# Optimization experiments

Measured on AMD Instinct MI355X. Metric: run time of the kernel, lower is better.

## Reference

```python
import jax, jax.numpy as jnp
import numpy as np

ALPHA = 1.702   # SwiGLU alpha
LIMIT = 7.0     # swiglu_limit clamp
EPS = 1e-5      # RMSNorm eps
TOPK = 4        # experts_per_token
CHUNK = 8       # token chunk for gathered-weight einsum (bounds memory)


def _swiglu(h):
    # h: (..., 2*I) with interleaved [glu, linear] pairs
    g = jnp.minimum(h[..., ::2], LIMIT)
    l = jnp.clip(h[..., 1::2], -LIMIT, LIMIT)
    return g * jax.nn.sigmoid(ALPHA * g) * (l + 1.0)


def setup_inputs() -> dict:
    key = jax.random.key(0)
    ks = jax.random.split(key, 5)
    T, H, I, E = 1024, 1024, 1024, 64
    s = 0.02
    return {
        "x": jax.random.normal(ks[0], (T, H), jnp.float32),
        "norm_scale": jnp.ones((H,), jnp.float32),
        "gate_w": jax.random.normal(ks[1], (E, H), jnp.float32) * s,
        "gate_b": jnp.zeros((E,), jnp.float32),
        "mlp1_w": jax.random.normal(ks[2], (E, 2 * I, H), jnp.float32) * s,
        "mlp1_b": jnp.zeros((E, 2 * I), jnp.float32),
        "mlp2_w": jax.random.normal(ks[3], (E, H, I), jnp.float32) * s,
        "mlp2_b": jnp.zeros((E, H), jnp.float32),
    }


def reference(x, norm_scale, gate_w, gate_b, mlp1_w, mlp1_b, mlp2_w, mlp2_b):
    # RMSNorm (fp32 math)
    t = x * jax.lax.rsqrt(jnp.mean(x * x, axis=-1, keepdims=True) + EPS) * norm_scale
    # gating: top-k over gate logits, softmax over the k selected
    logits = t @ gate_w.T + gate_b                     # (T, E)
    vals, idx = jax.lax.top_k(logits, TOPK)            # sorted desc, matches torch.topk(sorted=True)
    ew = jax.nn.softmax(vals, axis=-1)                 # (T, k)

    T_, H = t.shape
    nc = T_ // CHUNK

    @jax.checkpoint
    def per_chunk(args):
        xc, ic, wc = args                              # (C,H), (C,k), (C,k)
        h = jnp.einsum('bekh,bh->bek', mlp1_w[ic], xc) + mlp1_b[ic]   # (C,k,2I)
        h = _swiglu(h)                                                 # (C,k,I)
        o = jnp.einsum('behi,bei->beh', mlp2_w[ic], h) + mlp2_b[ic]    # (C,k,H)
        return jnp.einsum('beh,be->bh', o, wc)                         # (C,H)

    out = jax.lax.map(per_chunk, (t.reshape(nc, CHUNK, H),
                                  idx.reshape(nc, CHUNK, TOPK),
                                  ew.reshape(nc, CHUNK, TOPK)))
    return x + out.reshape(T_, H)
```

## Files before the change

### kernel.cpp

```cpp
#include <hip/hip_runtime.h>
#include <hip/hip_bf16.h>

#define GLOBAL_AS __attribute__((address_space(1)))
#define LDS_AS    __attribute__((address_space(3)))

typedef __bf16 bf16x8 __attribute__((ext_vector_type(8)));
typedef float  f32x4v __attribute__((ext_vector_type(4)));

__device__ __forceinline__ unsigned short f2bf(float f) {
    union { float f; unsigned int u; } a; a.f = f;
    unsigned int u = a.u;
    u += 0x7FFFu + ((u >> 16) & 1u);
    return (unsigned short)(u >> 16);
}

__global__ __launch_bounds__(256) void k_rmsnorm(const float* __restrict__ x,
        const float* __restrict__ sc, float* __restrict__ t32,
        unsigned short* __restrict__ t16)
{
    const int t = blockIdx.x, tid = threadIdx.x;
    const float4 v = ((const float4*)(x + (size_t)t * 1024))[tid];
    float ss = v.x*v.x + v.y*v.y + v.z*v.z + v.w*v.w;
    #pragma unroll
    for (int s = 32; s; s >>= 1) ss += __shfl_xor(ss, s, 64);
    __shared__ float red[4];
    if ((tid & 63) == 0) red[tid >> 6] = ss;
    __syncthreads();
    const float tot = red[0] + red[1] + red[2] + red[3];
    const float rs = rsqrtf(tot * (1.0f / 1024.0f) + 1e-5f);
    const float4 s4 = ((const float4*)sc)[tid];
    float4 o;
    o.x = v.x * rs * s4.x; o.y = v.y * rs * s4.y;
    o.z = v.z * rs * s4.z; o.w = v.w * rs * s4.w;
    ((float4*)(t32 + (size_t)t * 1024))[tid] = o;
    uint2 p;
    p.x = (unsigned)f2bf(o.x) | ((unsigned)f2bf(o.y) << 16);
    p.y = (unsigned)f2bf(o.z) | ((unsigned)f2bf(o.w) << 16);
    ((uint2*)(t16 + (size_t)t * 1024))[tid] = p;
}

__global__ __launch_bounds__(64) void k_gate(const float* __restrict__ t32,
        const float* __restrict__ gw, const float* __restrict__ gb,
        int* __restrict__ idx, float* __restrict__ ew)
{
    const int t = blockIdx.x, tid = threadIdx.x;
    __shared__ float4 tl[256];
    __shared__ float lg[64];
    const float4* xr = (const float4*)(t32 + (size_t)t * 1024);
    #pragma unroll
    for (int i = 0; i < 4; ++i) tl[i * 64 + tid] = xr[i * 64 + tid];
    __syncthreads();
    const float4* w4 = (const float4*)(gw + (size_t)tid * 1024);
    float acc = gb[tid];
    for (int k = 0; k < 256; ++k) {
        const float4 a = tl[k], b = w4[k];
        acc += a.x*b.x; acc += a.y*b.y; acc += a.z*b.z; acc += a.w*b.w;
    }
    lg[tid] = acc;
    __syncthreads();
    if (tid == 0) {
        unsigned long long taken = 0ull;
        float vals[4]; int ids[4];
        for (int k = 0; k < 4; ++k) {
            float bv = -3.0e38f; int bi = 0;
            for (int e = 0; e < 64; ++e) {
                if ((taken >> e) & 1ull) continue;
                if (lg[e] > bv) { bv = lg[e]; bi = e; }
            }
            taken |= 1ull << bi; vals[k] = bv; ids[k] = bi;
        }
        float ex[4], s = 0.0f;
        for (int k = 0; k < 4; ++k) { ex[k] = expf(vals[k] - vals[0]); s += ex[k]; }
        const float inv = 1.0f / s;
        for (int k = 0; k < 4; ++k) { idx[t*4+k] = ids[k]; ew[t*4+k] = ex[k] * inv; }
    }
}

__global__ __launch_bounds__(256) void k_bucket(const int* __restrict__ idx,
        const float* __restrict__ ewv, int* __restrict__ eoff,
        int* __restrict__ slot_token, float* __restrict__ slot_ew,
        int* __restrict__ token_slots)
{
    __shared__ int cnt[64], cur[64];
    const int tid = threadIdx.x;
    if (tid < 64) cnt[tid] = 0;
    __syncthreads();
    for (int p = tid; p < 4096; p += 256) atomicAdd(&cnt[idx[p]], 1);
    __syncthreads();
    if (tid == 0) {
        int s = 0;
        for (int e = 0; e < 64; ++e) { eoff[e] = s; cur[e] = s; s += cnt[e]; }
        eoff[64] = s;
    }
    __syncthreads();
    for (int p = tid; p < 4096; p += 256) {
        const int e = idx[p];
        const int s = atomicAdd(&cur[e], 1);
        slot_token[s] = p >> 2;
        slot_ew[s] = ewv[p];
        token_slots[p] = s;
    }
}

template<int MODE>
__global__ __launch_bounds__(256, 2) void k_gemm(
        const float* __restrict__ W, const float* __restrict__ Bias,
        const unsigned short* __restrict__ A,
        const int* __restrict__ eoff, const int* __restrict__ slot_token,
        const float* __restrict__ slot_ew,
        unsigned short* __restrict__ act_out, float* __restrict__ o_buf)
{
    constexpr int NPE = (MODE == 0) ? 2048 : 1024;
    const int e  = blockIdx.y;
    const int nt = blockIdx.x;
    const int off = eoff[e];
    const int count = eoff[e + 1] - off;
    if (count == 0) return;
    const int tid = threadIdx.x;
    const int wv = tid >> 6, l = tid & 63;
    const int wm = wv >> 1, wn = wv & 1;

    __shared__ unsigned char lds[2][32768];

    const float* Wb = W + (size_t)e * NPE * 1024 + (size_t)nt * 128 * 1024;

    for (int mt = 0; mt * 128 < count; ++mt) {
        const unsigned char* asrc[4];
        #pragma unroll
        for (int i = 0; i < 4; ++i) {
            const int chunk = wv * 4 + i;
            const int row = chunk * 8 + (l >> 3);
            const int colbyte = ((l & 7) ^ (l >> 3)) << 4;
            int arow;
            if (MODE == 0) {
                int slot = off + mt * 128 + row;
                const int smax = off + count - 1;
                if (slot > smax) slot = smax;
                arow = slot_token[slot];
            } else {
                arow = off + mt * 128 + row;
            }
            asrc[i] = (const unsigned char*)A + (size_t)arow * 2048 + colbyte;
        }

        f32x4v acc[4][4];
        #pragma unroll
        for (int m = 0; m < 4; ++m)
            #pragma unroll
            for (int n = 0; n < 4; ++n)
                acc[m][n] = f32x4v{0.f, 0.f, 0.f, 0.f};

        float4 bv[8];

        #pragma unroll
        for (int i = 0; i < 4; ++i)
            __builtin_amdgcn_global_load_lds((const GLOBAL_AS void*)asrc[i],
                (LDS_AS void*)&lds[0][(wv * 4 + i) * 1024], 16, 0, 0);
        #pragma unroll
        for (int it = 0; it < 8; ++it) {
            const int fid = it * 256 + tid;
            bv[it] = *(const float4*)(Wb + (size_t)(fid >> 4) * 1024 + (fid & 15) * 4);
        }
        #pragma unroll
        for (int it = 0; it < 8; ++it) {
            const int fid = it * 256 + tid;
            const int row = fid >> 4, c4 = fid & 15;
            uint2 p;
            p.x = (unsigned)f2bf(bv[it].x) | ((unsigned)f2bf(bv[it].y) << 16);
            p.y = (unsigned)f2bf(bv[it].z) | ((unsigned)f2bf(bv[it].w) << 16);
            *(uint2*)(&lds[0][16384 + row * 128 + ((c4 * 8) ^ ((row & 7) << 4))]) = p;
        }
        __syncthreads();

        int buf = 0;
        for (int kt = 0; kt < 16; ++kt) {
            const bool pf = (kt < 15);
            if (pf) {
                #pragma unroll
                for (int i = 0; i < 4; ++i)
                    __builtin_amdgcn_global_load_lds(
                        (const GLOBAL_AS void*)(asrc[i] + (kt + 1) * 128),
                        (LDS_AS void*)&lds[buf ^ 1][(wv * 4 + i) * 1024], 16, 0, 0);
                #pragma unroll
                for (int it = 0; it < 8; ++it) {
                    const int fid = it * 256 + tid;
                    bv[it] = *(const float4*)(Wb + (size_t)(fid >> 4) * 1024
                                              + (kt + 1) * 64 + (fid & 15) * 4);
                }
            }
            #pragma unroll
            for (int kk = 0; kk < 2; ++kk) {
                bf16x8 af[4], bfr[4];
                #pragma unroll
                for (int m = 0; m < 4; ++m) {
                    const int row = wm * 64 + m * 16 + (l & 15);
                    af[m] = *(const bf16x8*)(&lds[buf][row * 128 +
                              ((kk * 64 + ((l >> 4) * 16)) ^ ((row & 7) << 4))]);
                }
                #pragma unroll
                for (int n = 0; n < 4; ++n) {
                    const int row = wn * 64 + n * 16 + (l & 15);
                    bfr[n] = *(const bf16x8*)(&lds[buf][16384 + row * 128 +
                              ((kk * 64 + ((l >> 4) * 16)) ^ ((row & 7) << 4))]);
                }
                #pragma unroll
                for (int m = 0; m < 4; ++m)
                    #pragma unroll
                    for (int n = 0; n < 4; ++n)
                        acc[m][n] = __builtin_amdgcn_mfma_f32_16x16x32_bf16(
                                        af[m], bfr[n], acc[m][n], 0, 0, 0);
            }
            if (pf) {
                #pragma unroll
                for (int it = 0; it < 8; ++it) {
                    const int fid = it * 256 + tid;
                    const int row = fid >> 4, c4 = fid & 15;
                    uint2 p;
                    p.x = (unsigned)f2bf(bv[it].x) | ((unsigned)f2bf(bv[it].y) << 16);
                    p.y = (unsigned)f2bf(bv[it].z) | ((unsigned)f2bf(bv[it].w) << 16);
                    *(uint2*)(&lds[buf ^ 1][16384 + row * 128 +
                              ((c4 * 8) ^ ((row & 7) << 4))]) = p;
                }
            }
            __syncthreads();
            buf ^= 1;
        }

        #pragma unroll
        for (int m = 0; m < 4; ++m) {
            #pragma unroll
            for (int n = 0; n < 4; ++n) {
                #pragma unroll
                for (int j = 0; j < 4; ++j) {
                    const int row  = wm * 64 + m * 16 + (l >> 4) * 4 + j;
                    const int coll = wn * 64 + n * 16 + (l & 15);
                    const int gn = nt * 128 + coll;
                    const int gm = mt * 128 + row;
                    if (MODE == 0) {
                        float v = acc[m][n][j] + Bias[(size_t)e * NPE + gn];
                        const float partner = __shfl_xor(v, 1, 64);
                        if (!(l & 1) && gm < count) {
                            const float g  = fminf(v, 7.0f);
                            const float lv = fminf(fmaxf(partner, -7.0f), 7.0f);
                            const float r  = g / (1.0f + expf(-1.702f * g)) * (lv + 1.0f);
                            act_out[(size_t)(off + gm) * 1024 + (gn >> 1)] = f2bf(r);
                        }
                    } else {
                        if (gm < count) {
                            const int slot = off + gm;
                            const float v = acc[m][n][j] + Bias[(size_t)e * NPE + gn];
                            o_buf[(size_t)slot * 1024 + gn] = v * slot_ew[slot];
                        }
                    }
                }
            }
        }
    }
}

__global__ __launch_bounds__(256) void k_combine(const float* __restrict__ x,
        const float* __restrict__ o_buf, const int* __restrict__ tslot,
        float* __restrict__ out)
{
    const int t = blockIdx.x, tid = threadIdx.x;
    float4 r = ((const float4*)(x + (size_t)t * 1024))[tid];
    #pragma unroll
    for (int k = 0; k < 4; ++k) {
        const int s = tslot[t * 4 + k];
        const float4 o = ((const float4*)(o_buf + (size_t)s * 1024))[tid];
        r.x += o.x; r.y += o.y; r.z += o.z; r.w += o.w;
    }
    ((float4*)(out + (size_t)t * 1024))[tid] = r;
}

extern "C" void kernel_launch(void* const* d_in, const int* in_sizes, int n_in,
                              void* d_out, int out_size, void* d_ws, size_t ws_size,
                              hipStream_t stream)
{
    const float* x   = (const float*)d_in[0];
    const float* nsc = (const float*)d_in[1];
    const float* gw  = (const float*)d_in[2];
    const float* gb  = (const float*)d_in[3];
    const float* w1  = (const float*)d_in[4];
    const float* b1  = (const float*)d_in[5];
    const float* w2  = (const float*)d_in[6];
    const float* b2  = (const float*)d_in[7];
    float* out = (float*)d_out;
    (void)in_sizes; (void)n_in; (void)out_size; (void)ws_size;

    char* ws = (char*)d_ws;
    float*          t32   = (float*)(ws);
    unsigned short* t16   = (unsigned short*)(ws + (4u  << 20));
    unsigned short* act   = (unsigned short*)(ws + (6u  << 20));
    float*          obuf  = (float*)(ws + (16u << 20));
    int*            idx   = (int*)  (ws + (32u << 20));
    float*          ew    = (float*)(ws + (32u << 20) + 1 * 65536);
    int*            stok  = (int*)  (ws + (32u << 20) + 2 * 65536);
    float*          sew   = (float*)(ws + (32u << 20) + 3 * 65536);
    int*            tslot = (int*)  (ws + (32u << 20) + 4 * 65536);
    int*            eoff  = (int*)  (ws + (32u << 20) + 5 * 65536);

    k_rmsnorm<<<1024, 256, 0, stream>>>(x, nsc, t32, t16);
    k_gate   <<<1024,  64, 0, stream>>>(t32, gw, gb, idx, ew);
    k_bucket <<<   1, 256, 0, stream>>>(idx, ew, eoff, stok, sew, tslot);
    k_gemm<0><<<dim3(16, 64), 256, 0, stream>>>(w1, b1, t16, eoff, stok, sew, act, nullptr);
    k_gemm<1><<<dim3( 8, 64), 256, 0, stream>>>(w2, b2, act, eoff, stok, sew, nullptr, obuf);
    k_combine<<<1024, 256, 0, stream>>>(x, obuf, tslot, out);
}
```

Baseline: 294.7 us.

## Deepen GEMM weight prefetch pipeline and parallelize gating top-k across waves

The expert GEMM main loop is unrolled by two and keeps two register buffers of fp32 weights, so weight loads run two K-tiles ahead. Explicit sched_barrier and s_waitcnt calls control the overlap of the A-tile DMA into LDS, the B loads, the MFMA work and the LDS writes. The gating kernel moves to 256 threads with a split-K dot product and a wave-wide shuffle/ballot top-k in place of a serial single-thread scan. Manual bf16 rounding is replaced by native __bf16 conversion. The risks are higher register pressure from the doubled prefetch buffers, and redundant clamped loads past the last K tile.

```diff
diff --git a/kernel.cpp b/kernel.cpp
--- a/kernel.cpp
+++ b/kernel.cpp
@@ -5,18 +5,12 @@
 #define LDS_AS    __attribute__((address_space(3)))
 
 typedef __bf16 bf16x8 __attribute__((ext_vector_type(8)));
+typedef __bf16 bf16x4 __attribute__((ext_vector_type(4)));
 typedef float  f32x4v __attribute__((ext_vector_type(4)));
-
-__device__ __forceinline__ unsigned short f2bf(float f) {
-    union { float f; unsigned int u; } a; a.f = f;
-    unsigned int u = a.u;
-    u += 0x7FFFu + ((u >> 16) & 1u);
-    return (unsigned short)(u >> 16);
-}
 
 __global__ __launch_bounds__(256) void k_rmsnorm(const float* __restrict__ x,
         const float* __restrict__ sc, float* __restrict__ t32,
-        unsigned short* __restrict__ t16)
+        __bf16* __restrict__ t16)
 {
     const int t = blockIdx.x, tid = threadIdx.x;
     const float4 v = ((const float4*)(x + (size_t)t * 1024))[tid];
@@ -33,46 +27,48 @@
     o.x = v.x * rs * s4.x; o.y = v.y * rs * s4.y;
     o.z = v.z * rs * s4.z; o.w = v.w * rs * s4.w;
     ((float4*)(t32 + (size_t)t * 1024))[tid] = o;
-    uint2 p;
-    p.x = (unsigned)f2bf(o.x) | ((unsigned)f2bf(o.y) << 16);
-    p.y = (unsigned)f2bf(o.z) | ((unsigned)f2bf(o.w) << 16);
-    ((uint2*)(t16 + (size_t)t * 1024))[tid] = p;
-}
-
-__global__ __launch_bounds__(64) void k_gate(const float* __restrict__ t32,
+    bf16x4 p;
+    p[0] = (__bf16)o.x; p[1] = (__bf16)o.y; p[2] = (__bf16)o.z; p[3] = (__bf16)o.w;
+    ((bf16x4*)(t16 + (size_t)t * 1024))[tid] = p;
+}
+
+__global__ __launch_bounds__(256) void k_gate(const float* __restrict__ t32,
         const float* __restrict__ gw, const float* __restrict__ gb,
         int* __restrict__ idx, float* __restrict__ ew)
 {
     const int t = blockIdx.x, tid = threadIdx.x;
     __shared__ float4 tl[256];
-    __shared__ float lg[64];
-    const float4* xr = (const float4*)(t32 + (size_t)t * 1024);
-    #pragma unroll
-    for (int i = 0; i < 4; ++i) tl[i * 64 + tid] = xr[i * 64 + tid];
-    __syncthreads();
-    const float4* w4 = (const float4*)(gw + (size_t)tid * 1024);
-    float acc = gb[tid];
-    for (int k = 0; k < 256; ++k) {
-        const float4 a = tl[k], b = w4[k];
-        acc += a.x*b.x; acc += a.y*b.y; acc += a.z*b.z; acc += a.w*b.w;
-    }
-    lg[tid] = acc;
-    __syncthreads();
-    if (tid == 0) {
-        unsigned long long taken = 0ull;
+    __shared__ float part[4][64];
+    tl[tid] = ((const float4*)(t32 + (size_t)t * 1024))[tid];
+    __syncthreads();
+    const int q = tid >> 6, e = tid & 63;
+    const float4* w4 = (const float4*)(gw + (size_t)e * 1024 + q * 256);
+    const float4* a4 = &tl[q * 64];
+    float acc = 0.0f;
+    #pragma unroll 8
+    for (int i = 0; i < 64; ++i) {
+        const float4 a = a4[i], b = w4[i];
+        acc += a.x*b.x + a.y*b.y + a.z*b.z + a.w*b.w;
+    }
+    part[q][e] = acc;
+    __syncthreads();
+    if (tid < 64) {
+        float cur = part[0][tid] + part[1][tid] + part[2][tid] + part[3][tid] + gb[tid];
         float vals[4]; int ids[4];
+        #pragma unroll
         for (int k = 0; k < 4; ++k) {
-            float bv = -3.0e38f; int bi = 0;
-            for (int e = 0; e < 64; ++e) {
-                if ((taken >> e) & 1ull) continue;
-                if (lg[e] > bv) { bv = lg[e]; bi = e; }
-            }
-            taken |= 1ull << bi; vals[k] = bv; ids[k] = bi;
+            float m = cur;
+            #pragma unroll
+            for (int s = 32; s; s >>= 1) m = fmaxf(m, __shfl_xor(m, s, 64));
+            const unsigned long long b = __ballot(cur == m);
+            const int bi = __ffsll(b) - 1;
+            vals[k] = m; ids[k] = bi;
+            if (tid == bi) cur = -3.0e38f;
         }
         float ex[4], s = 0.0f;
+        #pragma unroll
         for (int k = 0; k < 4; ++k) { ex[k] = expf(vals[k] - vals[0]); s += ex[k]; }
-        const float inv = 1.0f / s;
-        for (int k = 0; k < 4; ++k) { idx[t*4+k] = ids[k]; ew[t*4+k] = ex[k] * inv; }
+        if (tid < 4) { idx[t * 4 + tid] = ids[tid]; ew[t * 4 + tid] = ex[tid] / s; }
     }
 }
 
@@ -105,10 +101,10 @@
 template<int MODE>
 __global__ __launch_bounds__(256, 2) void k_gemm(
         const float* __restrict__ W, const float* __restrict__ Bias,
-        const unsigned short* __restrict__ A,
+        const __bf16* __restrict__ A,
         const int* __restrict__ eoff, const int* __restrict__ slot_token,
         const float* __restrict__ slot_ew,
-        unsigned short* __restrict__ act_out, float* __restrict__ o_buf)
+        __bf16* __restrict__ act_out, float* __restrict__ o_buf)
 {
     constexpr int NPE = (MODE == 0) ? 2048 : 1024;
     const int e  = blockIdx.y;
@@ -120,9 +116,63 @@
     const int wv = tid >> 6, l = tid & 63;
     const int wm = wv >> 1, wn = wv & 1;
 
-    __shared__ unsigned char lds[2][32768];
+    __shared__ __attribute__((aligned(16))) unsigned char lds[2][32768];
 
     const float* Wb = W + (size_t)e * NPE * 1024 + (size_t)nt * 128 * 1024;
+
+#define DMA_A(sbuf, kt) do {                                                   \
+    const int kk_ = (kt) > 15 ? 15 : (kt);                                     \
+    _Pragma("unroll")                                                          \
+    for (int i_ = 0; i_ < 4; ++i_)                                             \
+        __builtin_amdgcn_global_load_lds(                                      \
+            (const GLOBAL_AS void*)(asrc[i_] + kk_ * 128),                     \
+            (LDS_AS void*)&lds[sbuf][(wv * 4 + i_) * 1024], 16, 0, 0);         \
+    } while (0)
+
+#define LOAD_B(dst, kt) do {                                                   \
+    const int kk_ = (kt) > 15 ? 15 : (kt);                                     \
+    _Pragma("unroll")                                                          \
+    for (int it_ = 0; it_ < 8; ++it_) {                                        \
+        const int fid_ = it_ * 256 + tid;                                      \
+        dst[it_] = *(const float4*)(Wb + (size_t)(fid_ >> 4) * 1024            \
+                                    + kk_ * 64 + (fid_ & 15) * 4);             \
+    } } while (0)
+
+#define WRITE_B(src, sbuf) do {                                                \
+    _Pragma("unroll")                                                          \
+    for (int it_ = 0; it_ < 8; ++it_) {                                        \
+        const int fid_ = it_ * 256 + tid;                                      \
+        const int row_ = fid_ >> 4, c4_ = fid_ & 15;                           \
+        bf16x4 p_;                                                             \
+        p_[0] = (__bf16)src[it_].x; p_[1] = (__bf16)src[it_].y;                \
+        p_[2] = (__bf16)src[it_].z; p_[3] = (__bf16)src[it_].w;                \
+        *(bf16x4*)(&lds[sbuf][16384 + row_ * 128 +                             \
+                   ((c4_ * 8) ^ ((row_ & 7) << 4))]) = p_;                     \
+    } } while (0)
+
+#define COMPUTE(cbuf) do {                                                     \
+    _Pragma("unroll")                                                          \
+    for (int kk_ = 0; kk_ < 2; ++kk_) {                                        \
+        bf16x8 af_[4], bf_[4];                                                 \
+        _Pragma("unroll")                                                      \
+        for (int m_ = 0; m_ < 4; ++m_) {                                       \
+            const int row_ = wm * 64 + m_ * 16 + (l & 15);                     \
+            af_[m_] = *(const bf16x8*)(&lds[cbuf][row_ * 128 +                 \
+                      ((kk_ * 64 + ((l >> 4) * 16)) ^ ((row_ & 7) << 4))]);    \
+        }                                                                      \
+        _Pragma("unroll")                                                      \
+        for (int n_ = 0; n_ < 4; ++n_) {                                       \
+            const int row_ = wn * 64 + n_ * 16 + (l & 15);                     \
+            bf_[n_] = *(const bf16x8*)(&lds[cbuf][16384 + row_ * 128 +         \
+                      ((kk_ * 64 + ((l >> 4) * 16)) ^ ((row_ & 7) << 4))]);    \
+        }                                                                      \
+        _Pragma("unroll")                                                      \
+        for (int m_ = 0; m_ < 4; ++m_)                                         \
+            _Pragma("unroll")                                                  \
+            for (int n_ = 0; n_ < 4; ++n_)                                     \
+                acc[m_][n_] = __builtin_amdgcn_mfma_f32_16x16x32_bf16(         \
+                                  af_[m_], bf_[n_], acc[m_][n_], 0, 0, 0);     \
+    } } while (0)
 
     for (int mt = 0; mt * 128 < count; ++mt) {
         const unsigned char* asrc[4];
@@ -150,80 +200,39 @@
             for (int n = 0; n < 4; ++n)
                 acc[m][n] = f32x4v{0.f, 0.f, 0.f, 0.f};
 
-        float4 bv[8];
-
-        #pragma unroll
-        for (int i = 0; i < 4; ++i)
-            __builtin_amdgcn_global_load_lds((const GLOBAL_AS void*)asrc[i],
-                (LDS_AS void*)&lds[0][(wv * 4 + i) * 1024], 16, 0, 0);
-        #pragma unroll
-        for (int it = 0; it < 8; ++it) {
-            const int fid = it * 256 + tid;
-            bv[it] = *(const float4*)(Wb + (size_t)(fid >> 4) * 1024 + (fid & 15) * 4);
-        }
-        #pragma unroll
-        for (int it = 0; it < 8; ++it) {
-            const int fid = it * 256 + tid;
-            const int row = fid >> 4, c4 = fid & 15;
-            uint2 p;
-            p.x = (unsigned)f2bf(bv[it].x) | ((unsigned)f2bf(bv[it].y) << 16);
-            p.y = (unsigned)f2bf(bv[it].z) | ((unsigned)f2bf(bv[it].w) << 16);
-            *(uint2*)(&lds[0][16384 + row * 128 + ((c4 * 8) ^ ((row & 7) << 4))]) = p;
-        }
-        __syncthreads();
-
-        int buf = 0;
-        for (int kt = 0; kt < 16; ++kt) {
-            const bool pf = (kt < 15);
-            if (pf) {
-                #pragma unroll
-                for (int i = 0; i < 4; ++i)
-                    __builtin_amdgcn_global_load_lds(
-                        (const GLOBAL_AS void*)(asrc[i] + (kt + 1) * 128),
-                        (LDS_AS void*)&lds[buf ^ 1][(wv * 4 + i) * 1024], 16, 0, 0);
-                #pragma unroll
-                for (int it = 0; it < 8; ++it) {
-                    const int fid = it * 256 + tid;
-                    bv[it] = *(const float4*)(Wb + (size_t)(fid >> 4) * 1024
-                                              + (kt + 1) * 64 + (fid & 15) * 4);
-                }
-            }
-            #pragma unroll
-            for (int kk = 0; kk < 2; ++kk) {
-                bf16x8 af[4], bfr[4];
-                #pragma unroll
-                for (int m = 0; m < 4; ++m) {
-                    const int row = wm * 64 + m * 16 + (l & 15);
-                    af[m] = *(const bf16x8*)(&lds[buf][row * 128 +
-                              ((kk * 64 + ((l >> 4) * 16)) ^ ((row & 7) << 4))]);
-                }
-                #pragma unroll
-                for (int n = 0; n < 4; ++n) {
-                    const int row = wn * 64 + n * 16 + (l & 15);
-                    bfr[n] = *(const bf16x8*)(&lds[buf][16384 + row * 128 +
-                              ((kk * 64 + ((l >> 4) * 16)) ^ ((row & 7) << 4))]);
-                }
-                #pragma unroll
-                for (int m = 0; m < 4; ++m)
-                    #pragma unroll
-                    for (int n = 0; n < 4; ++n)
-                        acc[m][n] = __builtin_amdgcn_mfma_f32_16x16x32_bf16(
-                                        af[m], bfr[n], acc[m][n], 0, 0, 0);
-            }
-            if (pf) {
-                #pragma unroll
-                for (int it = 0; it < 8; ++it) {
-                    const int fid = it * 256 + tid;
-                    const int row = fid >> 4, c4 = fid & 15;
-                    uint2 p;
-                    p.x = (unsigned)f2bf(bv[it].x) | ((unsigned)f2bf(bv[it].y) << 16);
-                    p.y = (unsigned)f2bf(bv[it].z) | ((unsigned)f2bf(bv[it].w) << 16);
-                    *(uint2*)(&lds[buf ^ 1][16384 + row * 128 +
-                              ((c4 * 8) ^ ((row & 7) << 4))]) = p;
-                }
-            }
-            __syncthreads();
-            buf ^= 1;
+        float4 bvA[8], bvB[8];
+
+        DMA_A(0, 0);
+        __builtin_amdgcn_sched_barrier(0);
+        LOAD_B(bvA, 0);
+        WRITE_B(bvA, 0);
+        __builtin_amdgcn_sched_barrier(0);
+        LOAD_B(bvA, 1);
+        asm volatile("s_waitcnt lgkmcnt(0)" ::: "memory");
+        __builtin_amdgcn_sched_barrier(0);
+        __builtin_amdgcn_s_barrier();
+
+        #pragma unroll 1
+        for (int p = 0; p < 8; ++p) {
+            const int kt0 = 2 * p, kt1 = 2 * p + 1;
+            DMA_A(1, kt0 + 1);
+            __builtin_amdgcn_sched_barrier(0);
+            LOAD_B(bvB, kt0 + 2);
+            __builtin_amdgcn_sched_barrier(0);
+            COMPUTE(0);
+            WRITE_B(bvA, 1);
+            asm volatile("s_waitcnt vmcnt(8) lgkmcnt(0)" ::: "memory");
+            __builtin_amdgcn_sched_barrier(0);
+            __builtin_amdgcn_s_barrier();
+            DMA_A(0, kt1 + 1);
+            __builtin_amdgcn_sched_barrier(0);
+            LOAD_B(bvA, kt1 + 2);
+            __builtin_amdgcn_sched_barrier(0);
+            COMPUTE(1);
+            WRITE_B(bvB, 0);
+            asm volatile("s_waitcnt vmcnt(8) lgkmcnt(0)" ::: "memory");
+            __builtin_amdgcn_sched_barrier(0);
+            __builtin_amdgcn_s_barrier();
         }
 
         #pragma unroll
@@ -243,7 +252,7 @@
                             const float g  = fminf(v, 7.0f);
                             const float lv = fminf(fmaxf(partner, -7.0f), 7.0f);
                             const float r  = g / (1.0f + expf(-1.702f * g)) * (lv + 1.0f);
-                            act_out[(size_t)(off + gm) * 1024 + (gn >> 1)] = f2bf(r);
+                            act_out[(size_t)(off + gm) * 1024 + (gn >> 1)] = (__bf16)r;
                         }
                     } else {
                         if (gm < count) {
@@ -256,6 +265,10 @@
             }
         }
     }
+#undef DMA_A
+#undef LOAD_B
+#undef WRITE_B
+#undef COMPUTE
 }
 
 __global__ __launch_bounds__(256) void k_combine(const float* __restrict__ x,
@@ -289,19 +302,19 @@
     (void)in_sizes; (void)n_in; (void)out_size; (void)ws_size;
 
     char* ws = (char*)d_ws;
-    float*          t32   = (float*)(ws);
-    unsigned short* t16   = (unsigned short*)(ws + (4u  << 20));
-    unsigned short* act   = (unsigned short*)(ws + (6u  << 20));
-    float*          obuf  = (float*)(ws + (16u << 20));
-    int*            idx   = (int*)  (ws + (32u << 20));
-    float*          ew    = (float*)(ws + (32u << 20) + 1 * 65536);
-    int*            stok  = (int*)  (ws + (32u << 20) + 2 * 65536);
-    float*          sew   = (float*)(ws + (32u << 20) + 3 * 65536);
-    int*            tslot = (int*)  (ws + (32u << 20) + 4 * 65536);
-    int*            eoff  = (int*)  (ws + (32u << 20) + 5 * 65536);
+    float*  t32   = (float*)(ws);
+    __bf16* t16   = (__bf16*)(ws + (4u  << 20));
+    __bf16* act   = (__bf16*)(ws + (6u  << 20));
+    float*  obuf  = (float*)(ws + (16u << 20));
+    int*    idx   = (int*)  (ws + (34u << 20));
+    float*  ew    = (float*)(ws + (34u << 20) + 1 * 65536);
+    int*    stok  = (int*)  (ws + (34u << 20) + 2 * 65536);
+    float*  sew   = (float*)(ws + (34u << 20) + 3 * 65536);
+    int*    tslot = (int*)  (ws + (34u << 20) + 4 * 65536);
+    int*    eoff  = (int*)  (ws + (34u << 20) + 5 * 65536);
 
     k_rmsnorm<<<1024, 256, 0, stream>>>(x, nsc, t32, t16);
-    k_gate   <<<1024,  64, 0, stream>>>(t32, gw, gb, idx, ew);
+    k_gate   <<<1024, 256, 0, stream>>>(t32, gw, gb, idx, ew);
     k_bucket <<<   1, 256, 0, stream>>>(idx, ew, eoff, stok, sew, tslot);
     k_gemm<0><<<dim3(16, 64), 256, 0, stream>>>(w1, b1, t16, eoff, stok, sew, act, nullptr);
     k_gemm<1><<<dim3( 8, 64), 256, 0, stream>>>(w2, b2, act, eoff, stok, sew, nullptr, obuf);
```

After: 287.1 us. 2.6% less time.
